# Performance work log

Measured on AMD Instinct MI355X. Metric: run time of the kernel, lower is better.

Reference implementation:

```python
import jax, jax.numpy as jnp
import numpy as np

H = 8  # heads hardcoded in LightGFormer


def layernorm(x, g, b, eps=1e-5):
    m = x.mean(-1, keepdims=True)
    v = ((x - m) ** 2).mean(-1, keepdims=True)
    return (x - m) / jnp.sqrt(v + eps) * g + b


def setup_inputs() -> dict:
    key = jax.random.key(0)
    B, N, D, L = 16, 512, 256, 4
    Dff = 4 * D
    ks = jax.random.split(key, 12)

    def w(k, shape, scale=0.02):
        return jax.random.normal(k, shape, jnp.float32) * scale

    return {
        "input": w(ks[0], (B, N, D), 1.0),
        "input_v": w(ks[1], (B, N, D), 1.0),
        "pos_emb": w(ks[2], (N, D)),
        "Wq": w(ks[3], (L, D, D)), "bq": jnp.zeros((L, D), jnp.float32),
        "Wk": w(ks[4], (L, D, D)), "bk": jnp.zeros((L, D), jnp.float32),
        "Wv": w(ks[5], (L, D, D)), "bv": jnp.zeros((L, D), jnp.float32),
        "Wo": w(ks[6], (L, D, D)), "bo": jnp.zeros((L, D), jnp.float32),
        "W1": w(ks[7], (L, D, Dff)), "b1": jnp.zeros((L, Dff), jnp.float32),
        "W2": w(ks[8], (L, Dff // 2, D // 2)), "b2": jnp.zeros((L, D // 2), jnp.float32),
        "g1": jnp.ones((L, D), jnp.float32), "be1": jnp.zeros((L, D), jnp.float32),
        "g2": jnp.ones((L, D), jnp.float32), "be2": jnp.zeros((L, D), jnp.float32),
        "gf": jnp.ones((D,), jnp.float32), "bf": jnp.zeros((D,), jnp.float32),
        "mask": jax.random.randint(ks[9], (N, N), 0, 2) > 0,
    }


def reference(input, input_v, pos_emb, Wq, bq, Wk, bk, Wv, bv, Wo, bo,
              W1, b1, W2, b2, g1, be1, g2, be2, gf, bf, mask):
    B, N, D = input.shape
    L = Wq.shape[0]
    dk = D // H
    scale = 1.0 / float(np.sqrt(dk))

    x = input + pos_emb[None]       # learned positional encoding
    xv = input_v + pos_emb[None]    # values stream (never updated across layers)

    for i in range(L):
        # --- self-attention: queries/keys from x, values from xv ---
        q = (x @ Wq[i] + bq[i]).reshape(B, N, H, dk)
        k = (x @ Wk[i] + bk[i]).reshape(B, N, H, dk)
        v = (xv @ Wv[i] + bv[i]).reshape(B, N, H, dk)
        att = jnp.einsum('bqhd,bkhd->bhqk', q, k) * scale
        if i % 2 == 1:  # odd layers use the mask (Lightformer alternation)
            att = jnp.where(mask[None, None], -jnp.inf, att)
        att = jax.nn.softmax(att, axis=-1)
        o = jnp.einsum('bhqk,bkhd->bqhd', att, v).reshape(B, N, D)
        o = o @ Wo[i] + bo[i]
        x = layernorm(x + o, g1[i], be1[i])
        # --- FFN with grouped second linear: [.., 2, 2D] @ [2D, D/2] ---
        h = jax.nn.gelu(x @ W1[i] + b1[i], approximate=False)
        h = (h.reshape(B, N, 2, 2 * D) @ W2[i] + b2[i]).reshape(B, N, D)
        x = layernorm(x + h, g2[i], be2[i])

    x = layernorm(x, gf, bf)  # final attention_norm
    return x
```

## Files before the change

kernel.cpp:

```cpp
#include <hip/hip_runtime.h>
#include <hip/hip_bf16.h>
#include <math.h>

#define BDIM 16
#define NSEQ 512
#define DMODEL 256
#define NLAYER 4
#define NHEAD 8
#define DK 32
#define DFF 1024
#define BN (BDIM * NSEQ)
#define ND (NSEQ * DMODEL)

typedef __bf16 bf16x8 __attribute__((ext_vector_type(8)));
typedef float floatx4 __attribute__((ext_vector_type(4)));
typedef unsigned uint32x2 __attribute__((ext_vector_type(2)));

static __device__ __forceinline__ unsigned short f2bf(float f) {
    unsigned u = __float_as_uint(f);
    unsigned r = (u + 0x7FFFu + ((u >> 16) & 1u)) >> 16;
    return (unsigned short)r;
}

static __device__ __forceinline__ void async_ld16(const unsigned short* g,
                                                  unsigned short* l) {
    __builtin_amdgcn_global_load_lds(
        (const __attribute__((address_space(1))) unsigned int*)g,
        (__attribute__((address_space(3))) unsigned int*)l, 16, 0, 0);
}

static __device__ __forceinline__ float gelu_f(float c) {
    float u = 0.7978845608028654f * (c + 0.044715f * c * c * c);
    return c * (1.f / (1.f + __expf(-2.f * u)));
}

__global__ void conv_all_kernel(const float* __restrict__ Wq, const float* __restrict__ Wk,
                                const float* __restrict__ Wv, const float* __restrict__ Wo,
                                const float* __restrict__ W1, const float* __restrict__ W2,
                                const int* __restrict__ mask,
                                unsigned short* __restrict__ wqT, unsigned short* __restrict__ wkT,
                                unsigned short* __restrict__ wvT, unsigned short* __restrict__ woT,
                                unsigned short* __restrict__ w1T, unsigned short* __restrict__ w2T,
                                unsigned* __restrict__ bits) {
    int blk = blockIdx.x, tid = threadIdx.x;
    if (blk < 4096) {
        int i = blk * 256 + tid;
        int sel = i >> 18;
        int j = i & 262143;
        int l = j >> 16, rem = j & 65535, kk = rem >> 8, n = rem & 255;
        const float* src = sel == 0 ? Wq : sel == 1 ? Wk : sel == 2 ? Wv : Wo;
        unsigned short* dst = sel == 0 ? wqT : sel == 1 ? wkT : sel == 2 ? wvT : woT;
        dst[(size_t)l * 65536 + n * 256 + kk] = f2bf(src[j]);
    } else if (blk < 8192) {
        int i = (blk - 4096) * 256 + tid;
        int l = i >> 18, rem = i & 262143, kk = rem >> 10, n = rem & 1023;
        w1T[(size_t)l * 262144 + (size_t)n * 256 + kk] = f2bf(W1[i]);
    } else if (blk < 9216) {
        int j = (blk - 8192) * 256 + tid;
        int l = j >> 16, rem = j & 65535, kk = rem >> 7, n = rem & 127;
        w2T[(size_t)l * 65536 + (size_t)n * 512 + kk] = f2bf(W2[j]);
    } else {
        int w = (blk - 9216) * 256 + tid;
        int r = w >> 4, wi = w & 15;
        const int* src = mask + r * NSEQ + wi * 32;
        unsigned acc = 0;
#pragma unroll
        for (int j = 0; j < 32; j++) acc |= (src[j] != 0 ? 1u : 0u) << j;
        bits[w] = acc;
    }
}

__global__ void add_pos_kernel(const float* __restrict__ in,
                               const float* __restrict__ inv,
                               const float* __restrict__ pos,
                               float* __restrict__ x,
                               unsigned short* __restrict__ xb,
                               unsigned short* __restrict__ xvb,
                               int total) {
    int i = blockIdx.x * blockDim.x + threadIdx.x;
    if (i < total) {
        float pe = pos[i % ND];
        float a = in[i] + pe;
        float b = inv[i] + pe;
        x[i] = a;
        xb[i] = f2bf(a);
        xvb[i] = f2bf(b);
    }
}

__global__ __launch_bounds__(256) void qkv_mfma_kernel(
        const unsigned short* __restrict__ xb,
        const unsigned short* __restrict__ xvb,
        const unsigned short* __restrict__ WqT, const unsigned short* __restrict__ WkT,
        const unsigned short* __restrict__ WvT,
        const float* __restrict__ bq, const float* __restrict__ bk,
        const float* __restrict__ bv,
        unsigned short* __restrict__ qo, unsigned short* __restrict__ ko,
        unsigned short* __restrict__ vo) {
    int proj = blockIdx.x >> 1;
    const unsigned short* A  = (proj == 2) ? xvb : xb;
    const unsigned short* Bt = (proj == 0) ? WqT : (proj == 1) ? WkT : WvT;
    const float* bias        = (proj == 0) ? bq  : (proj == 1) ? bk  : bv;
    unsigned short* Cb       = (proj == 0) ? qo  : (proj == 1) ? ko  : vo;
    float qscale = (proj == 0) ? 0.17677669529663687f : 1.f;

    __shared__ unsigned short As[128 * 32];
    __shared__ unsigned short Bs[128 * 32];
    int tid = threadIdx.x;
    int wave = tid >> 6, lane = tid & 63;
    int rowBase = blockIdx.y * 128, colBase = (blockIdx.x & 1) * 128;
    int m0w = (wave & 1) * 64, n0w = (wave >> 1) * 64;
    int lr = lane & 15, quad = lane >> 4;
    int qx = quad ^ (lr & 3);

    floatx4 acc[4][4];
#pragma unroll
    for (int mi = 0; mi < 4; mi++)
#pragma unroll
        for (int nj = 0; nj < 4; nj++) acc[mi][nj] = (floatx4)0.0f;

    for (int kt = 0; kt < DMODEL; kt += 32) {
#pragma unroll
        for (int t = 0; t < 2; t++) {
            int idx = t * 256 + tid;
            int row = idx >> 2, kv8 = ((idx ^ row) & 3) * 8;
            async_ld16(A + (size_t)(rowBase + row) * DMODEL + kt + kv8, &As[idx * 8]);
            async_ld16(Bt + (size_t)(colBase + row) * DMODEL + kt + kv8, &Bs[idx * 8]);
        }
        __syncthreads();
        bf16x8 af[4], bfr[4];
#pragma unroll
        for (int mi = 0; mi < 4; mi++)
            af[mi] = *(const bf16x8*)&As[(m0w + mi * 16 + lr) * 32 + qx * 8];
#pragma unroll
        for (int nj = 0; nj < 4; nj++)
            bfr[nj] = *(const bf16x8*)&Bs[(n0w + nj * 16 + lr) * 32 + qx * 8];
#pragma unroll
        for (int mi = 0; mi < 4; mi++)
#pragma unroll
            for (int nj = 0; nj < 4; nj++)
                acc[mi][nj] = __builtin_amdgcn_mfma_f32_16x16x32_bf16(
                    af[mi], bfr[nj], acc[mi][nj], 0, 0, 0);
        __syncthreads();
    }

#pragma unroll
    for (int mi = 0; mi < 4; mi++) {
#pragma unroll
        for (int r = 0; r < 4; r++) {
            int grow = rowBase + m0w + mi * 16 + quad * 4 + r;
#pragma unroll
            for (int nj = 0; nj < 4; nj++) {
                int gcol = colBase + n0w + nj * 16 + lr;
                float c = (acc[mi][nj][r] + bias[gcol]) * qscale;
                size_t off = ((size_t)((grow >> 9) * 8 + (gcol >> 5)) << 14)
                           + (size_t)(grow & 511) * 32 + (gcol & 31);
                Cb[off] = f2bf(c);
            }
        }
    }
}

__global__ __launch_bounds__(256) void gemm_mfma_kernel(
        const unsigned short* __restrict__ A,
        const unsigned short* __restrict__ Bt,
        const float* __restrict__ bias,
        unsigned short* __restrict__ Cb,
        int M, int K, int N, int act) {
    __shared__ unsigned short As[128 * 32];
    __shared__ unsigned short Bs[128 * 32];
    int tid = threadIdx.x;
    int wave = tid >> 6, lane = tid & 63;
    int rowBase = blockIdx.y * 128, colBase = blockIdx.x * 128;
    int m0w = (wave & 1) * 64, n0w = (wave >> 1) * 64;
    int lr = lane & 15, quad = lane >> 4;
    int qx = quad ^ (lr & 3);

    floatx4 acc[4][4];
#pragma unroll
    for (int mi = 0; mi < 4; mi++)
#pragma unroll
        for (int nj = 0; nj < 4; nj++) acc[mi][nj] = (floatx4)0.0f;

    for (int kt = 0; kt < K; kt += 32) {
#pragma unroll
        for (int t = 0; t < 2; t++) {
            int idx = t * 256 + tid;
            int row = idx >> 2, kv8 = ((idx ^ row) & 3) * 8;
            async_ld16(A + (size_t)(rowBase + row) * K + kt + kv8, &As[idx * 8]);
            async_ld16(Bt + (size_t)(colBase + row) * K + kt + kv8, &Bs[idx * 8]);
        }
        __syncthreads();
        bf16x8 af[4], bfr[4];
#pragma unroll
        for (int mi = 0; mi < 4; mi++)
            af[mi] = *(const bf16x8*)&As[(m0w + mi * 16 + lr) * 32 + qx * 8];
#pragma unroll
        for (int nj = 0; nj < 4; nj++)
            bfr[nj] = *(const bf16x8*)&Bs[(n0w + nj * 16 + lr) * 32 + qx * 8];
#pragma unroll
        for (int mi = 0; mi < 4; mi++)
#pragma unroll
            for (int nj = 0; nj < 4; nj++)
                acc[mi][nj] = __builtin_amdgcn_mfma_f32_16x16x32_bf16(
                    af[mi], bfr[nj], acc[mi][nj], 0, 0, 0);
        __syncthreads();
    }

#pragma unroll
    for (int mi = 0; mi < 4; mi++) {
#pragma unroll
        for (int r = 0; r < 4; r++) {
            int grow = rowBase + m0w + mi * 16 + quad * 4 + r;
#pragma unroll
            for (int nj = 0; nj < 4; nj++) {
                int gcol = colBase + n0w + nj * 16 + lr;
                float c = acc[mi][nj][r] + bias[gcol];
                if (act) c = gelu_f(c);
                Cb[(size_t)grow * N + gcol] = f2bf(c);
            }
        }
    }
}

__global__ __launch_bounds__(64) void wo_ln_kernel(
        const unsigned short* __restrict__ A,
        const unsigned short* __restrict__ Bt,
        const float* __restrict__ bias,
        const float* __restrict__ g, const float* __restrict__ be,
        float* __restrict__ xf, unsigned short* __restrict__ xb) {
    __shared__ unsigned short As[16 * 32];
    __shared__ unsigned short Bs[256 * 32];
    int tid = threadIdx.x;
    int l16 = tid & 15, quad = tid >> 4;
    int rowBase = blockIdx.x * 16;
    int qx = quad ^ (l16 & 3);

    floatx4 acc[16];
#pragma unroll
    for (int t = 0; t < 16; t++) acc[t] = (floatx4)0.0f;

    for (int kt = 0; kt < 256; kt += 32) {
        {
            int row = tid >> 2, kv8 = ((tid ^ row) & 3) * 8;
            async_ld16(A + (size_t)(rowBase + row) * 256 + kt + kv8, &As[tid * 8]);
        }
#pragma unroll
        for (int t = 0; t < 16; t++) {
            int idx = t * 64 + tid;
            int row = idx >> 2, kv8 = ((idx ^ row) & 3) * 8;
            async_ld16(Bt + (size_t)row * 256 + kt + kv8, &Bs[idx * 8]);
        }
        __syncthreads();
        bf16x8 af = *(const bf16x8*)&As[l16 * 32 + qx * 8];
#pragma unroll
        for (int t = 0; t < 16; t++) {
            bf16x8 bfr = *(const bf16x8*)&Bs[(t * 16 + l16) * 32 + qx * 8];
            acc[t] = __builtin_amdgcn_mfma_f32_16x16x32_bf16(af, bfr, acc[t], 0, 0, 0);
        }
        __syncthreads();
    }

    float bcol[16], gc[16], bec[16];
#pragma unroll
    for (int t = 0; t < 16; t++) {
        int c = t * 16 + l16;
        bcol[t] = bias[c]; gc[t] = g[c]; bec[t] = be[c];
    }
#pragma unroll
    for (int r = 0; r < 4; r++) {
        int grow = rowBase + quad * 4 + r;
        float v[16], s = 0.f, s2 = 0.f;
#pragma unroll
        for (int t = 0; t < 16; t++) {
            int c = t * 16 + l16;
            float val = acc[t][r] + bcol[t] + xf[(size_t)grow * 256 + c];
            v[t] = val; s += val; s2 += val * val;
        }
#pragma unroll
        for (int off = 1; off <= 8; off <<= 1) {
            s += __shfl_xor(s, off);
            s2 += __shfl_xor(s2, off);
        }
        float mean = s * (1.f / 256.f);
        float var = s2 * (1.f / 256.f) - mean * mean;
        float rstd = rsqrtf(var + 1e-5f);
#pragma unroll
        for (int t = 0; t < 16; t++) {
            int c = t * 16 + l16;
            float o = (v[t] - mean) * rstd * gc[t] + bec[t];
            xf[(size_t)grow * 256 + c] = o;
            xb[(size_t)grow * 256 + c] = f2bf(o);
        }
    }
}

__global__ __launch_bounds__(128) void ffn2_ln_kernel(
        const unsigned short* __restrict__ A,
        const unsigned short* __restrict__ Bt,
        const float* __restrict__ bias,
        const float* __restrict__ g, const float* __restrict__ be,
        float* __restrict__ xf, unsigned short* __restrict__ xb) {
    __shared__ unsigned short As[64 * 32];
    __shared__ unsigned short Bs[128 * 32];
    __shared__ float redS[64][2], redQ[64][2];
    int tid = threadIdx.x;
    int wave = tid >> 6, lane = tid & 63, l16 = lane & 15, quad = lane >> 4;
    int rowBase = blockIdx.x * 64;
    int n0w = wave * 64;
    int qx = quad ^ (l16 & 3);

    floatx4 acc[4][4];
#pragma unroll
    for (int mi = 0; mi < 4; mi++)
#pragma unroll
        for (int nj = 0; nj < 4; nj++) acc[mi][nj] = (floatx4)0.0f;

    for (int kt = 0; kt < 512; kt += 32) {
#pragma unroll
        for (int t = 0; t < 2; t++) {
            int idx = t * 128 + tid;
            int row = idx >> 2, kv8 = ((idx ^ row) & 3) * 8;
            async_ld16(A + (size_t)(rowBase + row) * 512 + kt + kv8, &As[idx * 8]);
        }
#pragma unroll
        for (int t = 0; t < 4; t++) {
            int idx = t * 128 + tid;
            int row = idx >> 2, kv8 = ((idx ^ row) & 3) * 8;
            async_ld16(Bt + (size_t)row * 512 + kt + kv8, &Bs[idx * 8]);
        }
        __syncthreads();
        bf16x8 af[4], bfr[4];
#pragma unroll
        for (int mi = 0; mi < 4; mi++)
            af[mi] = *(const bf16x8*)&As[(mi * 16 + l16) * 32 + qx * 8];
#pragma unroll
        for (int nj = 0; nj < 4; nj++)
            bfr[nj] = *(const bf16x8*)&Bs[(n0w + nj * 16 + l16) * 32 + qx * 8];
#pragma unroll
        for (int mi = 0; mi < 4; mi++)
#pragma unroll
            for (int nj = 0; nj < 4; nj++)
                acc[mi][nj] = __builtin_amdgcn_mfma_f32_16x16x32_bf16(
                    af[mi], bfr[nj], acc[mi][nj], 0, 0, 0);
        __syncthreads();
    }

#pragma unroll
    for (int mi = 0; mi < 4; mi++) {
#pragma unroll
        for (int r = 0; r < 4; r++) {
            int row = mi * 16 + quad * 4 + r;
            int grow = rowBase + row;
            int token = grow >> 1, dbase = (grow & 1) * 128;
            float s = 0.f, s2 = 0.f;
#pragma unroll
            for (int nj = 0; nj < 4; nj++) {
                int gcol = n0w + nj * 16 + l16;
                float val = acc[mi][nj][r] + bias[gcol]
                          + xf[(size_t)token * 256 + dbase + gcol];
                acc[mi][nj][r] = val;
                s += val; s2 += val * val;
            }
#pragma unroll
            for (int off = 1; off <= 8; off <<= 1) {
                s += __shfl_xor(s, off);
                s2 += __shfl_xor(s2, off);
            }
            if (l16 == 0) { redS[row][wave] = s; redQ[row][wave] = s2; }
        }
    }
    __syncthreads();

#pragma unroll
    for (int mi = 0; mi < 4; mi++) {
#pragma unroll
        for (int r = 0; r < 4; r++) {
            int row = mi * 16 + quad * 4 + r;
            int grow = rowBase + row;
            int token = grow >> 1, dbase = (grow & 1) * 128;
            float ts = redS[row][0] + redS[row][1] + redS[row ^ 1][0] + redS[row ^ 1][1];
            float tq = redQ[row][0] + redQ[row][1] + redQ[row ^ 1][0] + redQ[row ^ 1][1];
            float mean = ts * (1.f / 256.f);
            float var = tq * (1.f / 256.f) - mean * mean;
            float rstd = rsqrtf(var + 1e-5f);
#pragma unroll
            for (int nj = 0; nj < 4; nj++) {
                int gcol = n0w + nj * 16 + l16;
                int d = dbase + gcol;
                float o = (acc[mi][nj][r] - mean) * rstd * g[d] + be[d];
                xf[(size_t)token * 256 + d] = o;
                xb[(size_t)token * 256 + d] = f2bf(o);
            }
        }
    }
}

__global__ __launch_bounds__(256, 4) void attn_mfma_kernel(
        const unsigned short* __restrict__ q, const unsigned short* __restrict__ k,
        const unsigned short* __restrict__ v, unsigned short* __restrict__ o,
        const unsigned* __restrict__ mbits_g, int use_mask) {
    int bid = blockIdx.x;
    int qg = bid >> 7;
    int bh = bid & 127;
    int h = bh & 7, b = bh >> 3;
    int tid = threadIdx.x;

    __shared__ unsigned short Vs[2][NSEQ * 16];

    const unsigned short* kbase = k + (size_t)(b * 8 + h) * (NSEQ * DK);
    const unsigned short* vbase = v + (size_t)(b * 8 + h) * (NSEQ * DK);

#pragma unroll
    for (int db = 0; db < 2; db++) {
#pragma unroll
        for (int t = 0; t < 4; t++) {
            int c = t * 256 + tid;
            int kk = c >> 1, half = c & 1;
            async_ld16(vbase + (size_t)kk * 32 + db * 16 + half * 8,
                       &Vs[db][c * 8]);
        }
    }

    int wave = tid >> 6, lane = tid & 63, l16 = lane & 15, quad = lane >> 4;
    int qbase = qg * 64 + wave * 16;

    bf16x8 qf = *(const bf16x8*)(q + ((size_t)(b * 8 + h) * NSEQ + qbase + l16) * 32 + quad * 8);

    unsigned mw[16];
    if (use_mask) {
        const uint4* mr = (const uint4*)(mbits_g + (size_t)(qbase + l16) * 16);
#pragma unroll
        for (int w = 0; w < 4; w++) *(uint4*)&mw[w * 4] = mr[w];
    } else {
#pragma unroll
        for (int w = 0; w < 16; w++) mw[w] = 0;
    }
    __syncthreads();

    unsigned va0 = (unsigned)(size_t)&Vs[0][0] + (unsigned)(lane * 8);
    unsigned va1 = (unsigned)(size_t)&Vs[1][0] + (unsigned)(lane * 8);

    const unsigned short* kfrag = kbase + (size_t)l16 * DK + quad * 8;

    floatx4 oT0 = (floatx4)0.f, oT1 = (floatx4)0.f;
    float m_run = -INFINITY, l_part = 0.f;

    uint32x2 t00, t01, t10, t11;
#define TR_ISSUE(cc)                                                      \
    asm volatile("ds_read_b64_tr_b16 %0, %4\n\t"                          \
                 "ds_read_b64_tr_b16 %1, %4 offset:512\n\t"               \
                 "ds_read_b64_tr_b16 %2, %5\n\t"                          \
                 "ds_read_b64_tr_b16 %3, %5 offset:512"                   \
                 : "=&v"(t00), "=&v"(t01), "=&v"(t10), "=&v"(t11)         \
                 : "v"(va0 + (unsigned)((cc) * 1024)),                    \
                   "v"(va1 + (unsigned)((cc) * 1024)))
    TR_ISSUE(0);

    bf16x8 k0 = *(const bf16x8*)(kfrag);
    bf16x8 k1 = *(const bf16x8*)(kfrag + 16 * DK);

#pragma unroll
    for (int c = 0; c < 16; c++) {
        floatx4 s0 = __builtin_amdgcn_mfma_f32_16x16x32_bf16(k0, qf, (floatx4)0.f, 0, 0, 0);
        floatx4 s1 = __builtin_amdgcn_mfma_f32_16x16x32_bf16(k1, qf, (floatx4)0.f, 0, 0, 0);

        bf16x8 k0n, k1n;
        if (c < 15) {
            k0n = *(const bf16x8*)(kfrag + (size_t)((c + 1) * 32) * DK);
            k1n = *(const bf16x8*)(kfrag + (size_t)((c + 1) * 32 + 16) * DK);
        }

        float sv[8];
#pragma unroll
        for (int r = 0; r < 4; r++) { sv[r] = s0[r]; sv[4 + r] = s1[r]; }
        if (use_mask) {
            unsigned wb = mw[c];
#pragma unroll
            for (int r = 0; r < 4; r++) {
                if ((wb >> (quad * 4 + r)) & 1) sv[r] = -INFINITY;
                if ((wb >> (16 + quad * 4 + r)) & 1) sv[4 + r] = -INFINITY;
            }
        }
        float mx = fmaxf(fmaxf(fmaxf(sv[0], sv[1]), fmaxf(sv[2], sv[3])),
                         fmaxf(fmaxf(sv[4], sv[5]), fmaxf(sv[6], sv[7])));
        mx = fmaxf(mx, __shfl_xor(mx, 16));
        mx = fmaxf(mx, __shfl_xor(mx, 32));
        if (!__all(mx <= m_run)) {
            float mnew = fmaxf(m_run, mx);
            float corr = (m_run == mnew) ? 1.f : __expf(m_run - mnew);
            l_part *= corr;
            oT0 *= corr; oT1 *= corr;
            m_run = mnew;
        }
        float p[8];
#pragma unroll
        for (int j = 0; j < 8; j++) {
            float e = __expf(sv[j] - m_run);
            p[j] = (sv[j] > -INFINITY) ? e : 0.f;
            l_part += p[j];
        }
        union { bf16x8 v8; unsigned u[4]; } pf;
#pragma unroll
        for (int j = 0; j < 4; j++)
            asm("v_cvt_pk_bf16_f32 %0, %1, %2"
                : "=v"(pf.u[j]) : "v"(p[2 * j]), "v"(p[2 * j + 1]));

        asm volatile("s_waitcnt lgkmcnt(0)");
        __builtin_amdgcn_sched_barrier(0);
        union { bf16x8 v8; uint32x2 u[2]; } av0, av1;
        av0.u[0] = t00; av0.u[1] = t01;
        av1.u[0] = t10; av1.u[1] = t11;

        oT0 = __builtin_amdgcn_mfma_f32_16x16x32_bf16(av0.v8, pf.v8, oT0, 0, 0, 0);
        oT1 = __builtin_amdgcn_mfma_f32_16x16x32_bf16(av1.v8, pf.v8, oT1, 0, 0, 0);
        if (c < 15) TR_ISSUE(c + 1);
        k0 = k0n; k1 = k1n;
    }
#undef TR_ISSUE

    float l = l_part;
    l += __shfl_xor(l, 16);
    l += __shfl_xor(l, 32);
    float invl = (l > 0.f) ? 1.f / l : 0.f;

    unsigned short* orow = o + ((size_t)(b * NSEQ + qbase + l16)) * DMODEL + h * DK;
#pragma unroll
    for (int r = 0; r < 4; r++) {
        orow[quad * 4 + r]      = f2bf(oT0[r] * invl);
        orow[16 + quad * 4 + r] = f2bf(oT1[r] * invl);
    }
}

__global__ __launch_bounds__(256) void final_ln_kernel(
        const float* __restrict__ a,
        const float* __restrict__ g, const float* __restrict__ be,
        float* __restrict__ out) {
    int t = blockIdx.x;
    int d = threadIdx.x;
    size_t idx = (size_t)t * DMODEL + d;
    float v = a[idx];
    float s = v, s2 = v * v;
#pragma unroll
    for (int off = 32; off; off >>= 1) {
        s  += __shfl_xor(s, off);
        s2 += __shfl_xor(s2, off);
    }
    __shared__ float ws1[4], ws2[4];
    int wid = d >> 6;
    if ((d & 63) == 0) { ws1[wid] = s; ws2[wid] = s2; }
    __syncthreads();
    s  = ws1[0] + ws1[1] + ws1[2] + ws1[3];
    s2 = ws2[0] + ws2[1] + ws2[2] + ws2[3];
    float mean = s * (1.f / DMODEL);
    float var = s2 * (1.f / DMODEL) - mean * mean;
    float rstd = rsqrtf(var + 1e-5f);
    out[idx] = (v - mean) * rstd * g[d] + be[d];
}

extern "C" void kernel_launch(void* const* d_in, const int* in_sizes, int n_in,
                              void* d_out, int out_size, void* d_ws, size_t ws_size,
                              hipStream_t stream) {
    const float* input  = (const float*)d_in[0];
    const float* inputv = (const float*)d_in[1];
    const float* pos    = (const float*)d_in[2];
    const float* Wq = (const float*)d_in[3];
    const float* bq = (const float*)d_in[4];
    const float* Wk = (const float*)d_in[5];
    const float* bk = (const float*)d_in[6];
    const float* Wv = (const float*)d_in[7];
    const float* bv = (const float*)d_in[8];
    const float* Wo = (const float*)d_in[9];
    const float* bo = (const float*)d_in[10];
    const float* W1 = (const float*)d_in[11];
    const float* b1 = (const float*)d_in[12];
    const float* W2 = (const float*)d_in[13];
    const float* b2 = (const float*)d_in[14];
    const float* g1 = (const float*)d_in[15];
    const float* be1 = (const float*)d_in[16];
    const float* g2 = (const float*)d_in[17];
    const float* be2 = (const float*)d_in[18];
    const float* gf = (const float*)d_in[19];
    const float* bff = (const float*)d_in[20];
    const int* mask = (const int*)d_in[21];

    float* out = (float*)d_out;

    char* wsb = (char*)d_ws;
    float* x_f  = (float*)(wsb + ((size_t)0 << 20));
    unsigned short* x_b  = (unsigned short*)(wsb + ((size_t)8 << 20));
    unsigned short* xv_b = (unsigned short*)(wsb + ((size_t)12 << 20));
    unsigned short* qb_b = (unsigned short*)(wsb + ((size_t)16 << 20));
    unsigned short* kb_b = (unsigned short*)(wsb + ((size_t)20 << 20));
    unsigned short* vb_b = (unsigned short*)(wsb + ((size_t)24 << 20));
    unsigned short* ab_b = (unsigned short*)(wsb + ((size_t)28 << 20));
    unsigned short* h_b  = qb_b;
    unsigned short* wqT = (unsigned short*)(wsb + ((size_t)32 << 20));
    unsigned short* wkT = wqT + (size_t)4 * 65536;
    unsigned short* wvT = wkT + (size_t)4 * 65536;
    unsigned short* woT = wvT + (size_t)4 * 65536;
    unsigned short* w1T = woT + (size_t)4 * 65536;
    unsigned short* w2T = w1T + (size_t)4 * 262144;
    unsigned* mbits = (unsigned*)(wsb + ((size_t)37 << 20));

    const size_t TOK = (size_t)BN * DMODEL;

    conv_all_kernel<<<9248, 256, 0, stream>>>(Wq, Wk, Wv, Wo, W1, W2, mask,
                                              wqT, wkT, wvT, woT, w1T, w2T, mbits);
    add_pos_kernel<<<(int)((TOK + 255) / 256), 256, 0, stream>>>(
        input, inputv, pos, x_f, x_b, xv_b, (int)TOK);

    for (int i = 0; i < NLAYER; i++) {
        const unsigned short* WqT_i = wqT + (size_t)i * 65536;
        const unsigned short* WkT_i = wkT + (size_t)i * 65536;
        const unsigned short* WvT_i = wvT + (size_t)i * 65536;
        const unsigned short* WoT_i = woT + (size_t)i * 65536;
        const unsigned short* W1T_i = w1T + (size_t)i * 262144;
        const unsigned short* W2T_i = w2T + (size_t)i * 65536;

        qkv_mfma_kernel<<<dim3(6, 64), 256, 0, stream>>>(
            x_b, xv_b, WqT_i, WkT_i, WvT_i,
            bq + i * DMODEL, bk + i * DMODEL, bv + i * DMODEL,
            qb_b, kb_b, vb_b);

        attn_mfma_kernel<<<BDIM * NHEAD * 8, 256, 0, stream>>>(
            qb_b, kb_b, vb_b, ab_b, mbits, (i & 1));

        wo_ln_kernel<<<BN / 16, 64, 0, stream>>>(
            ab_b, WoT_i, bo + i * DMODEL,
            g1 + i * DMODEL, be1 + i * DMODEL, x_f, x_b);

        gemm_mfma_kernel<<<dim3(8, 64), 256, 0, stream>>>(
            x_b, W1T_i, b1 + i * DFF, h_b, BN, DMODEL, DFF, 1);

        ffn2_ln_kernel<<<(2 * BN) / 64, 128, 0, stream>>>(
            h_b, W2T_i, b2 + i * (DMODEL / 2),
            g2 + i * DMODEL, be2 + i * DMODEL, x_f, x_b);
    }

    final_ln_kernel<<<BN, DMODEL, 0, stream>>>(x_f, gf, bff, out);
}
```

Before: 454.6 us.

## Double-buffer LDS tiles with async prefetch in all GEMM kernels

Converts the four MFMA GEMM kernels (QKV, generic, Wo+LN, FFN2+LN) to double-buffered shared-memory tiles. The next K-tile is issued via async loads before computing on the current one, with explicit vmcnt waits and raw s_barrier in place of __syncthreads. The goal is to overlap global-to-LDS transfers with MFMA work. It doubles LDS usage, which may reduce occupancy. The hand-set vmcnt counts and the barrier removal in the single-wave Wo kernel are fragile if the number of loads per stage differs from what they assume.

```diff
diff --git a/kernel.cpp b/kernel.cpp
--- a/kernel.cpp
+++ b/kernel.cpp
@@ -104,8 +104,8 @@
     unsigned short* Cb       = (proj == 0) ? qo  : (proj == 1) ? ko  : vo;
     float qscale = (proj == 0) ? 0.17677669529663687f : 1.f;
 
-    __shared__ unsigned short As[128 * 32];
-    __shared__ unsigned short Bs[128 * 32];
+    __shared__ unsigned short As[2][128 * 32];
+    __shared__ unsigned short Bs[2][128 * 32];
     int tid = threadIdx.x;
     int wave = tid >> 6, lane = tid & 63;
     int rowBase = blockIdx.y * 128, colBase = (blockIdx.x & 1) * 128;
@@ -119,29 +119,43 @@
 #pragma unroll
         for (int nj = 0; nj < 4; nj++) acc[mi][nj] = (floatx4)0.0f;
 
-    for (int kt = 0; kt < DMODEL; kt += 32) {
+    auto stage = [&](int kt, int b) {
 #pragma unroll
         for (int t = 0; t < 2; t++) {
             int idx = t * 256 + tid;
             int row = idx >> 2, kv8 = ((idx ^ row) & 3) * 8;
-            async_ld16(A + (size_t)(rowBase + row) * DMODEL + kt + kv8, &As[idx * 8]);
-            async_ld16(Bt + (size_t)(colBase + row) * DMODEL + kt + kv8, &Bs[idx * 8]);
-        }
-        __syncthreads();
+            async_ld16(A + (size_t)(rowBase + row) * DMODEL + kt * 32 + kv8, &As[b][idx * 8]);
+            async_ld16(Bt + (size_t)(colBase + row) * DMODEL + kt * 32 + kv8, &Bs[b][idx * 8]);
+        }
+    };
+    stage(0, 0);
+
+    for (int kt = 0; kt < 8; kt++) {
+        int cur = kt & 1;
+        bool more = (kt < 7);
+        if (more) stage(kt + 1, cur ^ 1);
+        if (more) asm volatile("s_waitcnt vmcnt(4)");
+        else      asm volatile("s_waitcnt vmcnt(0)");
+        __builtin_amdgcn_s_barrier();
+        __builtin_amdgcn_sched_barrier(0);
         bf16x8 af[4], bfr[4];
 #pragma unroll
         for (int mi = 0; mi < 4; mi++)
-            af[mi] = *(const bf16x8*)&As[(m0w + mi * 16 + lr) * 32 + qx * 8];
+            af[mi] = *(const bf16x8*)&As[cur][(m0w + mi * 16 + lr) * 32 + qx * 8];
 #pragma unroll
         for (int nj = 0; nj < 4; nj++)
-            bfr[nj] = *(const bf16x8*)&Bs[(n0w + nj * 16 + lr) * 32 + qx * 8];
+            bfr[nj] = *(const bf16x8*)&Bs[cur][(n0w + nj * 16 + lr) * 32 + qx * 8];
 #pragma unroll
         for (int mi = 0; mi < 4; mi++)
 #pragma unroll
             for (int nj = 0; nj < 4; nj++)
                 acc[mi][nj] = __builtin_amdgcn_mfma_f32_16x16x32_bf16(
                     af[mi], bfr[nj], acc[mi][nj], 0, 0, 0);
-        __syncthreads();
+        if (more) {
+            asm volatile("s_waitcnt lgkmcnt(0)");
+            __builtin_amdgcn_sched_barrier(0);
+            __builtin_amdgcn_s_barrier();
+        }
     }
 
 #pragma unroll
@@ -167,14 +181,15 @@
         const float* __restrict__ bias,
         unsigned short* __restrict__ Cb,
         int M, int K, int N, int act) {
-    __shared__ unsigned short As[128 * 32];
-    __shared__ unsigned short Bs[128 * 32];
+    __shared__ unsigned short As[2][128 * 32];
+    __shared__ unsigned short Bs[2][128 * 32];
     int tid = threadIdx.x;
     int wave = tid >> 6, lane = tid & 63;
     int rowBase = blockIdx.y * 128, colBase = blockIdx.x * 128;
     int m0w = (wave & 1) * 64, n0w = (wave >> 1) * 64;
     int lr = lane & 15, quad = lane >> 4;
     int qx = quad ^ (lr & 3);
+    int NK = K >> 5;
 
     floatx4 acc[4][4];
 #pragma unroll
@@ -182,29 +197,43 @@
 #pragma unroll
         for (int nj = 0; nj < 4; nj++) acc[mi][nj] = (floatx4)0.0f;
 
-    for (int kt = 0; kt < K; kt += 32) {
+    auto stage = [&](int kt, int b) {
 #pragma unroll
         for (int t = 0; t < 2; t++) {
             int idx = t * 256 + tid;
             int row = idx >> 2, kv8 = ((idx ^ row) & 3) * 8;
-            async_ld16(A + (size_t)(rowBase + row) * K + kt + kv8, &As[idx * 8]);
-            async_ld16(Bt + (size_t)(colBase + row) * K + kt + kv8, &Bs[idx * 8]);
-        }
-        __syncthreads();
+            async_ld16(A + (size_t)(rowBase + row) * K + kt * 32 + kv8, &As[b][idx * 8]);
+            async_ld16(Bt + (size_t)(colBase + row) * K + kt * 32 + kv8, &Bs[b][idx * 8]);
+        }
+    };
+    stage(0, 0);
+
+    for (int kt = 0; kt < NK; kt++) {
+        int cur = kt & 1;
+        bool more = (kt < NK - 1);
+        if (more) stage(kt + 1, cur ^ 1);
+        if (more) asm volatile("s_waitcnt vmcnt(4)");
+        else      asm volatile("s_waitcnt vmcnt(0)");
+        __builtin_amdgcn_s_barrier();
+        __builtin_amdgcn_sched_barrier(0);
         bf16x8 af[4], bfr[4];
 #pragma unroll
         for (int mi = 0; mi < 4; mi++)
-            af[mi] = *(const bf16x8*)&As[(m0w + mi * 16 + lr) * 32 + qx * 8];
+            af[mi] = *(const bf16x8*)&As[cur][(m0w + mi * 16 + lr) * 32 + qx * 8];
 #pragma unroll
         for (int nj = 0; nj < 4; nj++)
-            bfr[nj] = *(const bf16x8*)&Bs[(n0w + nj * 16 + lr) * 32 + qx * 8];
+            bfr[nj] = *(const bf16x8*)&Bs[cur][(n0w + nj * 16 + lr) * 32 + qx * 8];
 #pragma unroll
         for (int mi = 0; mi < 4; mi++)
 #pragma unroll
             for (int nj = 0; nj < 4; nj++)
                 acc[mi][nj] = __builtin_amdgcn_mfma_f32_16x16x32_bf16(
                     af[mi], bfr[nj], acc[mi][nj], 0, 0, 0);
-        __syncthreads();
+        if (more) {
+            asm volatile("s_waitcnt lgkmcnt(0)");
+            __builtin_amdgcn_sched_barrier(0);
+            __builtin_amdgcn_s_barrier();
+        }
     }
 
 #pragma unroll
@@ -229,8 +258,8 @@
         const float* __restrict__ bias,
         const float* __restrict__ g, const float* __restrict__ be,
         float* __restrict__ xf, unsigned short* __restrict__ xb) {
-    __shared__ unsigned short As[16 * 32];
-    __shared__ unsigned short Bs[256 * 32];
+    __shared__ unsigned short As[2][16 * 32];
+    __shared__ unsigned short Bs[2][256 * 32];
     int tid = threadIdx.x;
     int l16 = tid & 15, quad = tid >> 4;
     int rowBase = blockIdx.x * 16;
@@ -240,25 +269,33 @@
 #pragma unroll
     for (int t = 0; t < 16; t++) acc[t] = (floatx4)0.0f;
 
-    for (int kt = 0; kt < 256; kt += 32) {
+    auto stage = [&](int kt, int b) {
         {
             int row = tid >> 2, kv8 = ((tid ^ row) & 3) * 8;
-            async_ld16(A + (size_t)(rowBase + row) * 256 + kt + kv8, &As[tid * 8]);
+            async_ld16(A + (size_t)(rowBase + row) * 256 + kt * 32 + kv8, &As[b][tid * 8]);
         }
 #pragma unroll
         for (int t = 0; t < 16; t++) {
             int idx = t * 64 + tid;
             int row = idx >> 2, kv8 = ((idx ^ row) & 3) * 8;
-            async_ld16(Bt + (size_t)row * 256 + kt + kv8, &Bs[idx * 8]);
-        }
-        __syncthreads();
-        bf16x8 af = *(const bf16x8*)&As[l16 * 32 + qx * 8];
+            async_ld16(Bt + (size_t)row * 256 + kt * 32 + kv8, &Bs[b][idx * 8]);
+        }
+    };
+    stage(0, 0);
+
+    for (int kt = 0; kt < 8; kt++) {
+        int cur = kt & 1;
+        bool more = (kt < 7);
+        if (more) stage(kt + 1, cur ^ 1);
+        if (more) asm volatile("s_waitcnt vmcnt(17)");
+        else      asm volatile("s_waitcnt vmcnt(0)");
+        __builtin_amdgcn_sched_barrier(0);
+        bf16x8 af = *(const bf16x8*)&As[cur][l16 * 32 + qx * 8];
 #pragma unroll
         for (int t = 0; t < 16; t++) {
-            bf16x8 bfr = *(const bf16x8*)&Bs[(t * 16 + l16) * 32 + qx * 8];
+            bf16x8 bfr = *(const bf16x8*)&Bs[cur][(t * 16 + l16) * 32 + qx * 8];
             acc[t] = __builtin_amdgcn_mfma_f32_16x16x32_bf16(af, bfr, acc[t], 0, 0, 0);
         }
-        __syncthreads();
     }
 
     float bcol[16], gc[16], bec[16];
@@ -301,8 +338,8 @@
         const float* __restrict__ bias,
         const float* __restrict__ g, const float* __restrict__ be,
         float* __restrict__ xf, unsigned short* __restrict__ xb) {
-    __shared__ unsigned short As[64 * 32];
-    __shared__ unsigned short Bs[128 * 32];
+    __shared__ unsigned short As[2][64 * 32];
+    __shared__ unsigned short Bs[2][128 * 32];
     __shared__ float redS[64][2], redQ[64][2];
     int tid = threadIdx.x;
     int wave = tid >> 6, lane = tid & 63, l16 = lane & 15, quad = lane >> 4;
@@ -316,34 +353,48 @@
 #pragma unroll
         for (int nj = 0; nj < 4; nj++) acc[mi][nj] = (floatx4)0.0f;
 
-    for (int kt = 0; kt < 512; kt += 32) {
+    auto stage = [&](int kt, int b) {
 #pragma unroll
         for (int t = 0; t < 2; t++) {
             int idx = t * 128 + tid;
             int row = idx >> 2, kv8 = ((idx ^ row) & 3) * 8;
-            async_ld16(A + (size_t)(rowBase + row) * 512 + kt + kv8, &As[idx * 8]);
+            async_ld16(A + (size_t)(rowBase + row) * 512 + kt * 32 + kv8, &As[b][idx * 8]);
         }
 #pragma unroll
         for (int t = 0; t < 4; t++) {
             int idx = t * 128 + tid;
             int row = idx >> 2, kv8 = ((idx ^ row) & 3) * 8;
-            async_ld16(Bt + (size_t)row * 512 + kt + kv8, &Bs[idx * 8]);
-        }
-        __syncthreads();
+            async_ld16(Bt + (size_t)row * 512 + kt * 32 + kv8, &Bs[b][idx * 8]);
+        }
+    };
+    stage(0, 0);
+
+    for (int kt = 0; kt < 16; kt++) {
+        int cur = kt & 1;
+        bool more = (kt < 15);
+        if (more) stage(kt + 1, cur ^ 1);
+        if (more) asm volatile("s_waitcnt vmcnt(6)");
+        else      asm volatile("s_waitcnt vmcnt(0)");
+        __builtin_amdgcn_s_barrier();
+        __builtin_amdgcn_sched_barrier(0);
         bf16x8 af[4], bfr[4];
 #pragma unroll
         for (int mi = 0; mi < 4; mi++)
-            af[mi] = *(const bf16x8*)&As[(mi * 16 + l16) * 32 + qx * 8];
+            af[mi] = *(const bf16x8*)&As[cur][(mi * 16 + l16) * 32 + qx * 8];
 #pragma unroll
         for (int nj = 0; nj < 4; nj++)
-            bfr[nj] = *(const bf16x8*)&Bs[(n0w + nj * 16 + l16) * 32 + qx * 8];
+            bfr[nj] = *(const bf16x8*)&Bs[cur][(n0w + nj * 16 + l16) * 32 + qx * 8];
 #pragma unroll
         for (int mi = 0; mi < 4; mi++)
 #pragma unroll
             for (int nj = 0; nj < 4; nj++)
                 acc[mi][nj] = __builtin_amdgcn_mfma_f32_16x16x32_bf16(
                     af[mi], bfr[nj], acc[mi][nj], 0, 0, 0);
-        __syncthreads();
+        if (more) {
+            asm volatile("s_waitcnt lgkmcnt(0)");
+            __builtin_amdgcn_sched_barrier(0);
+            __builtin_amdgcn_s_barrier();
+        }
     }
 
 #pragma unroll
```

Measured after the change: 462.4 us. No clear change (+1.7%).
